# Kernel optimization log

Measured on AMD Instinct MI355X. Metric: run time of the kernel, lower is better.

The kernel has to match this reference:

```python
import jax, jax.numpy as jnp
import numpy as np

UNIF_T = 2.0
EPS = 1e-12  # matches F.normalize default eps


def _l2norm(a):
    return a / jnp.maximum(jnp.linalg.norm(a, axis=-1, keepdims=True), EPS)


def setup_inputs() -> dict:
    key = jax.random.key(0)
    k1, k2, k3, k4 = jax.random.split(key, 4)
    n, d = 2048, 512
    Q, K = 3, 8192
    n_classes = 16
    x = jax.random.normal(k1, (n, d), dtype=jnp.float32)
    q_data = jax.random.normal(k2, (Q, K, d), dtype=jnp.float32)
    targets = jax.random.randint(k3, (n,), 0, n_classes, dtype=jnp.int64)
    q_targets = jax.random.randint(k4, (Q, K), 0, n_classes, dtype=jnp.int64)
    return {"x": x, "q_data": q_data, "targets": targets, "q_targets": q_targets, "order": 1}


def reference(x, q_data, targets, q_targets, order):
    # x: [n, d], q_data: [Q, K, d], targets: [n], q_targets: [Q, K]
    Q, K, _ = q_data.shape
    xn = _l2norm(x)
    qn = _l2norm(q_data)
    sim = jnp.einsum('nd,qkd->qnk', xn, qn)      # [Q, n, K]
    e = jnp.exp(-UNIF_T * (2.0 - 2.0 * sim))     # [Q, n, K]
    # mask[i, j] = targets[i] == q_targets[order, j]; masked entries of the
    # `order` queue are excluded from that row's mean.
    mask = targets[:, None] == q_targets[order][None, :]   # [n, K] bool
    total = e.sum(axis=(0, 2))                              # [n]
    masked_sum = jnp.where(mask, e[order], 0.0).sum(axis=1) # [n]
    count = (Q * K - mask.sum(axis=1)).astype(e.dtype)      # [n]
    loss = jnp.mean(jnp.log((total - masked_sum) / count))
    return loss
```

## Files before the change

### kernel.cpp

```cpp
#include <hip/hip_runtime.h>
#include <hip/hip_bf16.h>
#include <cstdint>
#include <cstddef>

#define N_ROWS 2048
#define DIM    512
#define QN     3
#define KQ     8192
#define NCOL   (QN * KQ)
#define NCLASS 16

#define BM 128
#define BN 128
#define BK 128
#define NBLK (NCOL / BN)

typedef __attribute__((ext_vector_type(4))) float f32x4;

__global__ __launch_bounds__(256) void norm_cast_kernel(
    const float* __restrict__ x, const float* __restrict__ q,
    unsigned char* __restrict__ xb, unsigned char* __restrict__ qb,
    float* __restrict__ out) {
    if (blockIdx.x == 0 && threadIdx.x == 0) out[0] = 0.f;
    int row = blockIdx.x * 4 + (threadIdx.x >> 6);
    int lane = threadIdx.x & 63;
    const float* src;
    unsigned char* dst;
    if (row < N_ROWS) {
        src = x + (size_t)row * DIM;
        dst = xb + (size_t)row * DIM;
    } else {
        src = q + (size_t)(row - N_ROWS) * DIM;
        dst = qb + (size_t)(row - N_ROWS) * DIM;
    }
    float4 v0 = ((const float4*)src)[lane * 2];
    float4 v1 = ((const float4*)src)[lane * 2 + 1];
    float ss = v0.x*v0.x + v0.y*v0.y + v0.z*v0.z + v0.w*v0.w
             + v1.x*v1.x + v1.y*v1.y + v1.z*v1.z + v1.w*v1.w;
    #pragma unroll
    for (int off = 1; off < 64; off <<= 1)
        ss += __shfl_xor(ss, off, 64);
    float inv = 16.0f / fmaxf(sqrtf(ss), 1e-12f);
    int w0 = __builtin_amdgcn_cvt_pk_fp8_f32(v0.x * inv, v0.y * inv, 0,  false);
    w0     = __builtin_amdgcn_cvt_pk_fp8_f32(v0.z * inv, v0.w * inv, w0, true);
    int w1 = __builtin_amdgcn_cvt_pk_fp8_f32(v1.x * inv, v1.y * inv, 0,  false);
    w1     = __builtin_amdgcn_cvt_pk_fp8_f32(v1.z * inv, v1.w * inv, w1, true);
    uint2 o; o.x = (unsigned)w0; o.y = (unsigned)w1;
    int r3 = (row >> 3) & 1;
    *(uint2*)(dst + ((lane * 8) ^ (r3 << 3))) = o;
}

__global__ __launch_bounds__(256) void gemm_epilogue_kernel(
    const unsigned char* __restrict__ Xb,
    const unsigned char* __restrict__ Qb,
    const int* __restrict__ targets,
    const int* __restrict__ q_targets,
    const int* __restrict__ order_p,
    float* __restrict__ P) {

    __shared__ unsigned char As[2][BM * BK];
    __shared__ unsigned char Bs[2][BN * BK];

    const int tid  = threadIdx.x;
    const int lane = tid & 63;
    const int wave = tid >> 6;
    const int wm = wave >> 1, wn = wave & 1;
    const int quad = lane >> 4;
    const int l15  = lane & 15;
    const int l7   = l15 & 7;
    const int l3   = (l15 >> 3) & 1;

    const int b    = blockIdx.x;
    const int xcd  = b & 7;
    const int g    = b >> 3;
    const int colb = (g >> 4) * 8 + xcd;
    const int rowb = g & 15;
    const int m0 = rowb * BM;
    const int n0 = colb * BN;

    f32x4 acc[4][4];
    #pragma unroll
    for (int i = 0; i < 4; i++)
        #pragma unroll
        for (int j = 0; j < 4; j++)
            acc[i][j] = (f32x4){0.f, 0.f, 0.f, 0.f};

    const int stR = (lane >> 3);
    const int stC = ((lane & 7) ^ stR) * 16;

    for (int kk = 0; kk < 2; kk++) {
        #pragma unroll
        for (int buf = 0; buf < 2; buf++) {
            const int k0 = kk * 256 + buf * 128;
            #pragma unroll
            for (int j = 0; j < 4; j++) {
                int chunk = wave * 4 + j;
                int R = chunk * 8 + stR;
                const unsigned char* ga = Xb + (size_t)(m0 + R) * DIM + k0 + stC;
                const unsigned char* gb = Qb + (size_t)(n0 + R) * DIM + k0 + stC;
                __builtin_amdgcn_global_load_lds(
                    (const __attribute__((address_space(1))) unsigned int*)ga,
                    (__attribute__((address_space(3))) unsigned int*)&As[buf][chunk * 1024 + lane * 16],
                    16, 0, 0);
                __builtin_amdgcn_global_load_lds(
                    (const __attribute__((address_space(1))) unsigned int*)gb,
                    (__attribute__((address_space(3))) unsigned int*)&Bs[buf][chunk * 1024 + lane * 16],
                    16, 0, 0);
            }
        }
        __syncthreads();

        #pragma unroll
        for (int buf = 0; buf < 2; buf++) {
            #pragma unroll
            for (int ks = 0; ks < BK; ks += 32) {
                const int sw = ((((ks >> 4) + (quad >> 1)) ^ l7) << 4)
                             + (((quad & 1) ^ l3) << 3);
                long a[4], bb[4];
                #pragma unroll
                for (int mt = 0; mt < 4; mt++)
                    a[mt] = *(const long*)&As[buf][(wm * 64 + mt * 16 + l15) * BK + sw];
                #pragma unroll
                for (int nt = 0; nt < 4; nt++)
                    bb[nt] = *(const long*)&Bs[buf][(wn * 64 + nt * 16 + l15) * BK + sw];
                #pragma unroll
                for (int mt = 0; mt < 4; mt++)
                    #pragma unroll
                    for (int nt = 0; nt < 4; nt++)
                        acc[mt][nt] = __builtin_amdgcn_mfma_f32_16x16x32_fp8_fp8(
                            a[mt], bb[nt], acc[mt][nt], 0, 0, 0);
            }
        }
        __syncthreads();
    }

    const int ord  = order_p[0];
    const int qIdx = colb / (KQ / BN);
    const bool isOrd = (qIdx == ord);
    const int kbase = n0 - qIdx * KQ;

    int qtv[4] = {0, 0, 0, 0};
    if (isOrd) {
        #pragma unroll
        for (int nt = 0; nt < 4; nt++)
            qtv[nt] = q_targets[ord * KQ + kbase + wn * 64 + nt * 16 + l15];
    }

    float* red = (float*)&As[0][0];

    #pragma unroll
    for (int mt = 0; mt < 4; mt++) {
        int rowl = wm * 64 + mt * 16 + quad * 4;
        int tg[4] = {0, 0, 0, 0};
        if (isOrd) {
            #pragma unroll
            for (int reg = 0; reg < 4; reg++) tg[reg] = targets[m0 + rowl + reg];
        }
        #pragma unroll
        for (int reg = 0; reg < 4; reg++) {
            float s = 0.f;
            #pragma unroll
            for (int nt = 0; nt < 4; nt++) {
                float v256 = acc[mt][nt][reg];
                float e = __expf(v256 * 0.015625f - 4.0f);
                if (isOrd && tg[reg] == qtv[nt]) e = 0.f;
                s += e;
            }
            s += __shfl_xor(s, 1, 64);
            s += __shfl_xor(s, 2, 64);
            s += __shfl_xor(s, 4, 64);
            s += __shfl_xor(s, 8, 64);
            if (l15 == 0)
                red[wn * 128 + rowl + reg] = s;
        }
    }
    __syncthreads();
    if (tid < 128)
        P[(size_t)colb * N_ROWS + m0 + tid] = red[tid] + red[128 + tid];
}

__global__ __launch_bounds__(256) void reduce_kernel(
    const float* __restrict__ P,
    const int* __restrict__ targets,
    const int* __restrict__ q_targets,
    const int* __restrict__ order_p,
    float* __restrict__ out) {
    __shared__ int hist[NCLASS];
    __shared__ float partial[4];
    int tid = threadIdx.x;
    int wave = tid >> 6, lane = tid & 63;
    if (tid < NCLASS) hist[tid] = 0;
    __syncthreads();
    int ord = order_p[0];

    int local[NCLASS];
    #pragma unroll
    for (int c = 0; c < NCLASS; c++) local[c] = 0;
    for (int i = tid; i < KQ; i += 256) {
        int v = q_targets[ord * KQ + i];
        #pragma unroll
        for (int c = 0; c < NCLASS; c++)
            local[c] += __popcll(__ballot(v == c));
    }
    if (lane == 0) {
        #pragma unroll
        for (int c = 0; c < NCLASS; c++)
            atomicAdd(&hist[c], local[c]);
    }
    __syncthreads();

    int r = blockIdx.x * 256 + tid;
    float total = 0.f;
    #pragma unroll 8
    for (int nb = 0; nb < NBLK; nb++)
        total += P[(size_t)nb * N_ROWS + r];
    float cnt = (float)(QN * KQ - hist[targets[r]]);
    float v = logf(total / cnt);

    #pragma unroll
    for (int off = 1; off < 64; off <<= 1)
        v += __shfl_xor(v, off, 64);
    if (lane == 0) partial[wave] = v;
    __syncthreads();
    if (tid == 0)
        atomicAdd(out, (partial[0] + partial[1] + partial[2] + partial[3])
                       * (1.0f / (float)N_ROWS));
}

extern "C" void kernel_launch(void* const* d_in, const int* in_sizes, int n_in,
                              void* d_out, int out_size, void* d_ws, size_t ws_size,
                              hipStream_t stream) {
    const float* x         = (const float*)d_in[0];
    const float* q         = (const float*)d_in[1];
    const int*   targets   = (const int*)d_in[2];
    const int*   q_targets = (const int*)d_in[3];
    const int*   order     = (const int*)d_in[4];
    float* out = (float*)d_out;

    char* ws = (char*)d_ws;
    float* P = (float*)ws;
    unsigned char* Xb = (unsigned char*)(ws + (size_t)NBLK * N_ROWS * 4);
    unsigned char* Qb = Xb + (size_t)N_ROWS * DIM;

    norm_cast_kernel<<<(N_ROWS + NCOL) / 4, 256, 0, stream>>>(x, q, Xb, Qb, out);

    gemm_epilogue_kernel<<<NBLK * (N_ROWS / BM), 256, 0, stream>>>(
        Xb, Qb, targets, q_targets, order, P);

    reduce_kernel<<<N_ROWS / 256, 256, 0, stream>>>(P, targets, q_targets, order, out);
}
```

Measured before the change: 175.4 us.

## Pipeline GEMM K-loop with BK=64 double-buffered prefetch overlapping compute

The GEMM main loop previously loaded two 128-wide K slices and then computed them, with a barrier between load and compute, so loads and MFMA work did not overlap. It now uses 64-wide K slices in a ping-pong buffer and issues the next slice's global-to-LDS load before computing the current one. LDS use halves, which may allow more resident blocks. The XOR swizzle in both the fp8 cast kernel and the LDS reads is redone for the 64-byte row pitch. In exchange there are twice as many barriers per tile, and the swizzle change risks bank conflicts or a layout mismatch.

```diff
diff --git a/kernel.cpp b/kernel.cpp
--- a/kernel.cpp
+++ b/kernel.cpp
@@ -12,7 +12,7 @@
 
 #define BM 128
 #define BN 128
-#define BK 128
+#define BK 64
 #define NBLK (NCOL / BN)
 
 typedef __attribute__((ext_vector_type(4))) float f32x4;
@@ -46,8 +46,8 @@
     int w1 = __builtin_amdgcn_cvt_pk_fp8_f32(v1.x * inv, v1.y * inv, 0,  false);
     w1     = __builtin_amdgcn_cvt_pk_fp8_f32(v1.z * inv, v1.w * inv, w1, true);
     uint2 o; o.x = (unsigned)w0; o.y = (unsigned)w1;
-    int r3 = (row >> 3) & 1;
-    *(uint2*)(dst + ((lane * 8) ^ (r3 << 3))) = o;
+    int r2 = (row >> 2) & 1;
+    *(uint2*)(dst + ((lane * 8) ^ (r2 << 3))) = o;
 }
 
 __global__ __launch_bounds__(256) void gemm_epilogue_kernel(
@@ -67,8 +67,8 @@
     const int wm = wave >> 1, wn = wave & 1;
     const int quad = lane >> 4;
     const int l15  = lane & 15;
-    const int l7   = l15 & 7;
-    const int l3   = (l15 >> 3) & 1;
+    const int l2   = l15 & 3;
+    const int lh   = (l15 >> 2) & 1;
 
     const int b    = blockIdx.x;
     const int xcd  = b & 7;
@@ -85,52 +85,55 @@
         for (int j = 0; j < 4; j++)
             acc[i][j] = (f32x4){0.f, 0.f, 0.f, 0.f};
 
-    const int stR = (lane >> 3);
-    const int stC = ((lane & 7) ^ stR) * 16;
-
-    for (int kk = 0; kk < 2; kk++) {
-        #pragma unroll
-        for (int buf = 0; buf < 2; buf++) {
-            const int k0 = kk * 256 + buf * 128;
-            #pragma unroll
-            for (int j = 0; j < 4; j++) {
-                int chunk = wave * 4 + j;
-                int R = chunk * 8 + stR;
-                const unsigned char* ga = Xb + (size_t)(m0 + R) * DIM + k0 + stC;
-                const unsigned char* gb = Qb + (size_t)(n0 + R) * DIM + k0 + stC;
-                __builtin_amdgcn_global_load_lds(
-                    (const __attribute__((address_space(1))) unsigned int*)ga,
-                    (__attribute__((address_space(3))) unsigned int*)&As[buf][chunk * 1024 + lane * 16],
-                    16, 0, 0);
-                __builtin_amdgcn_global_load_lds(
-                    (const __attribute__((address_space(1))) unsigned int*)gb,
-                    (__attribute__((address_space(3))) unsigned int*)&Bs[buf][chunk * 1024 + lane * 16],
-                    16, 0, 0);
-            }
-        }
-        __syncthreads();
-
-        #pragma unroll
-        for (int buf = 0; buf < 2; buf++) {
-            #pragma unroll
-            for (int ks = 0; ks < BK; ks += 32) {
-                const int sw = ((((ks >> 4) + (quad >> 1)) ^ l7) << 4)
-                             + (((quad & 1) ^ l3) << 3);
-                long a[4], bb[4];
-                #pragma unroll
-                for (int mt = 0; mt < 4; mt++)
-                    a[mt] = *(const long*)&As[buf][(wm * 64 + mt * 16 + l15) * BK + sw];
+    const int stR = (lane >> 2);
+    const int stG = ((lane & 3) ^ (stR & 3)) * 16;
+
+    auto stage = [&](int buf, int k0) {
+        #pragma unroll
+        for (int j = 0; j < 2; j++) {
+            int R = wave * 32 + j * 16 + stR;
+            const unsigned char* ga = Xb + (size_t)(m0 + R) * DIM + k0 + stG;
+            const unsigned char* gb = Qb + (size_t)(n0 + R) * DIM + k0 + stG;
+            __builtin_amdgcn_global_load_lds(
+                (const __attribute__((address_space(1))) unsigned int*)ga,
+                (__attribute__((address_space(3))) unsigned int*)
+                    &As[buf][wave * 2048 + j * 1024 + lane * 16],
+                16, 0, 0);
+            __builtin_amdgcn_global_load_lds(
+                (const __attribute__((address_space(1))) unsigned int*)gb,
+                (__attribute__((address_space(3))) unsigned int*)
+                    &Bs[buf][wave * 2048 + j * 1024 + lane * 16],
+                16, 0, 0);
+        }
+    };
+
+    auto compute = [&](int buf) {
+        #pragma unroll
+        for (int ks = 0; ks < BK; ks += 32) {
+            const int sw = ((((ks >> 4) + (quad >> 1)) ^ l2) << 4)
+                         + (((quad & 1) ^ lh) << 3);
+            long a[4], bb[4];
+            #pragma unroll
+            for (int mt = 0; mt < 4; mt++)
+                a[mt] = *(const long*)&As[buf][(wm * 64 + mt * 16 + l15) * BK + sw];
+            #pragma unroll
+            for (int nt = 0; nt < 4; nt++)
+                bb[nt] = *(const long*)&Bs[buf][(wn * 64 + nt * 16 + l15) * BK + sw];
+            #pragma unroll
+            for (int mt = 0; mt < 4; mt++)
                 #pragma unroll
                 for (int nt = 0; nt < 4; nt++)
-                    bb[nt] = *(const long*)&Bs[buf][(wn * 64 + nt * 16 + l15) * BK + sw];
-                #pragma unroll
-                for (int mt = 0; mt < 4; mt++)
-                    #pragma unroll
-                    for (int nt = 0; nt < 4; nt++)
-                        acc[mt][nt] = __builtin_amdgcn_mfma_f32_16x16x32_fp8_fp8(
-                            a[mt], bb[nt], acc[mt][nt], 0, 0, 0);
-            }
-        }
+                    acc[mt][nt] = __builtin_amdgcn_mfma_f32_16x16x32_fp8_fp8(
+                        a[mt], bb[nt], acc[mt][nt], 0, 0, 0);
+        }
+    };
+
+    stage(0, 0);
+    __syncthreads();
+    #pragma unroll
+    for (int i = 0; i < 8; i++) {
+        if (i < 7) stage((i + 1) & 1, (i + 1) * BK);
+        compute(i & 1);
         __syncthreads();
     }
 
```

After: 170.1 us. 1.03x faster.
